# Performance work log

Hardware: AMD Instinct MI355X
Metric: run time of the kernel (lower is better)

## Reference

```python
import jax, jax.numpy as jnp
import numpy as np
import math

B, M, V, C, HID, BIN, H, W = 2, 1024, 300, 128, 128, 256, 384, 512


def fibonacci_sphere(n):
    # generate_grasp_views: n approximately-uniform directions on the unit sphere
    i = np.arange(n, dtype=np.float64)
    phi = (np.sqrt(5.0) - 1.0) / 2.0
    z = (2.0 * i + 1.0) / n - 1.0
    r = np.sqrt(np.maximum(1.0 - z * z, 0.0))
    t = 2.0 * np.pi * i * phi
    v = np.stack([r * np.cos(t), r * np.sin(t), z], -1)
    return (v / np.linalg.norm(v, axis=-1, keepdims=True)).astype(np.float32)


def setup_inputs():
    key = jax.random.key(0)
    ks = jax.random.split(key, 24)
    seed_features = jax.random.normal(ks[0], (B, C, M), jnp.float32)
    token_sel_idx = jax.random.randint(ks[1], (B, M), 0, H * W)
    fx = 525.0
    Kmat = jnp.array([[fx, 0.0, W / 2.0], [0.0, fx, H / 2.0], [0.0, 0.0, 1.0]], jnp.float32)
    K = jnp.broadcast_to(Kmat, (B, 3, 3))
    depth_map = 0.2 + 0.8 * jax.random.uniform(ks[2], (B, 1, H, W), jnp.float32)
    depth_prob = jax.nn.softmax(jax.random.normal(ks[3], (B, BIN, H, W), jnp.float32), axis=1)
    view_dirs = jnp.asarray(fibonacci_sphere(V))

    def lin(k, fan_in, shape):
        s = 1.0 / np.sqrt(fan_in)
        return jax.random.uniform(k, shape, jnp.float32, -s, s)

    qin = C + 7  # seed_feat + ray(3) + normal(3) + uncert(1)
    params = dict(
        Wq1=lin(ks[4], qin, (qin, HID)), bq1=lin(ks[5], qin, (HID,)),
        Wq2=lin(ks[6], HID, (HID, HID)), bq2=lin(ks[7], HID, (HID,)),
        Wa1=lin(ks[8], 3, (3, HID)), ba1=lin(ks[9], 3, (HID,)),
        Wa2=lin(ks[10], HID, (HID, HID)), ba2=lin(ks[11], HID, (HID,)),
        Wb1=lin(ks[12], 3, (3, HID // 2)), bb1=lin(ks[13], 3, (HID // 2,)),
        Wb2=lin(ks[14], HID // 2, (HID // 2, 1)), bb2=lin(ks[15], HID // 2, (1,)),
        Wr1=lin(ks[16], HID, (HID, C)), br1=lin(ks[17], HID, (C,)),
        Wr2=lin(ks[18], C, (C, C)), br2=lin(ks[19], C, (C,)),
    )
    return dict(seed_features=seed_features, token_sel_idx=token_sel_idx, K=K,
                depth_map=depth_map, depth_prob=depth_prob, view_dirs=view_dirs, **params)


def _views_to_rot(views):
    # batch_viewpoint_params_to_matrix(-views, angle=0)
    axis_x = -views
    zero = jnp.zeros_like(axis_x[..., 0])
    axis_y = jnp.stack([-axis_x[..., 1], axis_x[..., 0], zero], -1)
    ny = jnp.linalg.norm(axis_y, axis=-1, keepdims=True)
    fallback = jnp.broadcast_to(jnp.array([0.0, 1.0, 0.0], views.dtype), axis_y.shape)
    axis_y = jnp.where(ny < 1e-8, fallback, axis_y / jnp.maximum(ny, 1e-8))
    axis_x = axis_x / jnp.maximum(jnp.linalg.norm(axis_x, axis=-1, keepdims=True), 1e-8)
    axis_z = jnp.cross(axis_x, axis_y)
    return jnp.stack([axis_x, axis_y, axis_z], -1)  # (B,M,3,3)


def _forward(seed_features, token_sel_idx, K, depth_map, depth_prob, view_dirs,
             Wq1, bq1, Wq2, bq2, Wa1, ba1, Wa2, ba2, Wb1, bb1, Wb2, bb2, Wr1, br1, Wr2, br2):
    depth_map = jax.lax.stop_gradient(depth_map)   # .detach() in torch
    depth_prob = jax.lax.stop_gradient(depth_prob)
    # --- backproject depth to xyz map (B,3,H,W) ---
    ys, xs = jnp.meshgrid(jnp.arange(H, dtype=jnp.float32), jnp.arange(W, dtype=jnp.float32), indexing='ij')
    fx = K[:, 0, 0][:, None, None, None]; fy = K[:, 1, 1][:, None, None, None]
    cx = K[:, 0, 2][:, None, None, None]; cy = K[:, 1, 2][:, None, None, None]
    z = depth_map
    x = (xs[None, None] - cx) / fx * z
    y = (ys[None, None] - cy) / fy * z
    xyz = jnp.concatenate([x, y, z], axis=1)
    # --- central-difference normal map with replicate pad ---
    dx = (xyz[:, :, :, 2:] - xyz[:, :, :, :-2])[:, :, 1:-1, :]
    dy = (xyz[:, :, 2:, :] - xyz[:, :, :-2, :])[:, :, :, 1:-1]
    n = jnp.cross(dx.transpose(0, 2, 3, 1), dy.transpose(0, 2, 3, 1))
    n = n / jnp.maximum(jnp.linalg.norm(n, axis=-1, keepdims=True), 1e-6)
    normal_map = jnp.pad(n.transpose(0, 3, 1, 2), ((0, 0), (0, 0), (1, 1), (1, 1)), mode='edge')
    # --- depth uncertainty: normalized entropy over bins ---
    p = jnp.maximum(depth_prob, 1e-8)
    uncert_map = jnp.clip(-(p * jnp.log(p)).sum(axis=1, keepdims=True) / math.log(BIN), 0.0, 1.0)
    # --- per-seed irregular gathers ---
    def gather(feat, idx):
        Bf, Cf = feat.shape[0], feat.shape[1]
        flat = feat.reshape(Bf, Cf, H * W)
        return jnp.take_along_axis(flat, jnp.broadcast_to(idx[:, None, :], (Bf, Cf, idx.shape[1])), axis=2)
    normal_bm3 = gather(normal_map, token_sel_idx).transpose(0, 2, 1)  # (B,M,3)
    uncert_bm1 = gather(uncert_map, token_sel_idx).transpose(0, 2, 1)  # (B,M,1)
    u = (token_sel_idx % W).astype(jnp.float32)
    v = (token_sel_idx // W).astype(jnp.float32)
    rx = (u - K[:, 0, 2][:, None]) / K[:, 0, 0][:, None]
    ry = (v - K[:, 1, 2][:, None]) / K[:, 1, 1][:, None]
    rays = jnp.stack([rx, ry, jnp.ones_like(rx)], -1)
    rays = rays / jnp.maximum(jnp.linalg.norm(rays, axis=-1, keepdims=True), 1e-12)
    normal_bm3 = normal_bm3 * (1.0 - uncert_bm1)
    # --- query / anchor / bias MLPs ---
    q_in = jnp.concatenate([seed_features.transpose(0, 2, 1), rays, normal_bm3, uncert_bm1], -1)
    q = jax.nn.relu(jax.nn.relu(q_in @ Wq1 + bq1) @ Wq2 + bq2)          # (B,M,HID)
    a = jax.nn.relu(view_dirs @ Wa1 + ba1) @ Wa2 + ba2                  # (V,HID)
    bias = (jax.nn.relu(view_dirs @ Wb1 + bb1) @ Wb2 + bb2)[:, 0]        # (V,)
    logits = jnp.einsum('bmh,vh->bmv', q, a) / jnp.sqrt(jnp.float32(HID)) + bias
    view_score = jax.nn.sigmoid(logits)                                  # (B,M,V)
    # --- top-1 view selection + gather xyz / rot / anchor feat ---
    top_inds = jnp.argmax(view_score, axis=-1)                           # (B,M)
    top_xyz = view_dirs[top_inds]                                        # (B,M,3)
    rot = _views_to_rot(top_xyz)                                         # (B,M,3,3)
    top_a = a[top_inds]                                                  # (B,M,HID)
    res = jax.nn.relu((q + top_a) @ Wr1 + br1) @ Wr2 + br2               # (B,M,C)
    res_feat = res.transpose(0, 2, 1)                                    # (B,C,M)
    return view_score, top_inds, top_xyz, rot, res_feat


def reference(seed_features, token_sel_idx, K, depth_map, depth_prob, view_dirs,
              Wq1, bq1, Wq2, bq2, Wa1, ba1, Wa2, ba2, Wb1, bb1, Wb2, bb2, Wr1, br1, Wr2, br2):
    return _forward(seed_features, token_sel_idx, K, depth_map, depth_prob, view_dirs,
                    Wq1, bq1, Wq2, bq2, Wa1, ba1, Wa2, ba2, Wb1, bb1, Wb2, bb2, Wr1, br1, Wr2, br2)
```

## Files before the change

kernel.cpp:

```cpp
#include <hip/hip_runtime.h>
#include <math.h>

#define B 2
#define M 1024
#define V 300
#define C 128
#define HID 128
#define BIN 256
#define H 384
#define W 512
#define QIN (C + 7)

__global__ __launch_bounds__(HID) void anchor_kernel(
    const float* __restrict__ view_dirs,
    const float* __restrict__ Wa1, const float* __restrict__ ba1,
    const float* __restrict__ Wa2, const float* __restrict__ ba2,
    const float* __restrict__ Wb1, const float* __restrict__ bb1,
    const float* __restrict__ Wb2, const float* __restrict__ bb2,
    float* __restrict__ a_out, float* __restrict__ bias_out) {
  const int v = blockIdx.x;
  const int t = threadIdx.x;
  __shared__ float h1[HID];
  __shared__ float hb[HID / 2];

  const float vd0 = view_dirs[v * 3 + 0];
  const float vd1 = view_dirs[v * 3 + 1];
  const float vd2 = view_dirs[v * 3 + 2];

  float h = vd0 * Wa1[0 * HID + t] + vd1 * Wa1[1 * HID + t] + vd2 * Wa1[2 * HID + t] + ba1[t];
  h1[t] = fmaxf(h, 0.0f);
  if (t < HID / 2) {
    float x = vd0 * Wb1[0 * 64 + t] + vd1 * Wb1[1 * 64 + t] + vd2 * Wb1[2 * 64 + t] + bb1[t];
    hb[t] = fmaxf(x, 0.0f);
  }
  __syncthreads();

  float acc = ba2[t];
#pragma unroll 8
  for (int k = 0; k < HID; ++k) acc += h1[k] * Wa2[k * HID + t];
  a_out[v * HID + t] = acc;

  if (t == 0) {
    float bacc = bb2[0];
    for (int k = 0; k < 64; ++k) bacc += hb[k] * Wb2[k];
    bias_out[v] = bacc;
  }
}

__global__ __launch_bounds__(128) void seed_kernel(
    const float* __restrict__ seed_features, const int* __restrict__ token_sel_idx,
    const float* __restrict__ Kmat, const float* __restrict__ depth_map,
    const float* __restrict__ depth_prob, const float* __restrict__ view_dirs,
    const float* __restrict__ Wq1, const float* __restrict__ bq1,
    const float* __restrict__ Wq2, const float* __restrict__ bq2,
    const float* __restrict__ Wr1, const float* __restrict__ br1,
    const float* __restrict__ Wr2, const float* __restrict__ br2,
    const float* __restrict__ a_ws, const float* __restrict__ bias_ws,
    float* __restrict__ out_view_score, float* __restrict__ out_top_inds,
    float* __restrict__ out_top_xyz, float* __restrict__ out_rot,
    float* __restrict__ out_res) {
  const int bm = blockIdx.x;
  const int b = bm / M;
  const int m = bm - b * M;
  const int t = threadIdx.x;

  __shared__ float qin_s[QIN + 1];
  __shared__ float hs[HID];
  __shared__ float qs[HID];
  __shared__ float red_v[128];
  __shared__ int   red_i[128];
  __shared__ float atop_s[HID];

  qin_s[t] = seed_features[((size_t)b * C + t) * M + m];

  const int idx = token_sel_idx[b * M + m];

  {
    const float* dp = depth_prob + (size_t)b * BIN * H * W + idx;
    float p0 = fmaxf(dp[(size_t)(2 * t + 0) * (H * W)], 1e-8f);
    float p1 = fmaxf(dp[(size_t)(2 * t + 1) * (H * W)], 1e-8f);
    red_v[t] = p0 * logf(p0) + p1 * logf(p1);
  }
  __syncthreads();
  for (int s = 64; s > 0; s >>= 1) {
    if (t < s) red_v[t] += red_v[t + s];
    __syncthreads();
  }

  if (t == 0) {
    float uncert = (-red_v[0]) / 5.5451774444795623f;
    uncert = fminf(fmaxf(uncert, 0.0f), 1.0f);

    const float fx = Kmat[b * 9 + 0], fy = Kmat[b * 9 + 4];
    const float cx = Kmat[b * 9 + 2], cy = Kmat[b * 9 + 5];
    const int w = idx % W;
    const int h = idx / W;
    const int hc = min(max(h, 1), H - 2);
    const int wc = min(max(w, 1), W - 2);

    const float* dm = depth_map + (size_t)b * H * W;
    const float zl = dm[hc * W + (wc - 1)];
    const float zr = dm[hc * W + (wc + 1)];
    const float zu = dm[(hc - 1) * W + wc];
    const float zd = dm[(hc + 1) * W + wc];

    const float dxx = (wc + 1 - cx) / fx * zr - (wc - 1 - cx) / fx * zl;
    const float dxy = (hc - cy) / fy * zr - (hc - cy) / fy * zl;
    const float dxz = zr - zl;
    const float dyx = (wc - cx) / fx * zd - (wc - cx) / fx * zu;
    const float dyy = (hc + 1 - cy) / fy * zd - (hc - 1 - cy) / fy * zu;
    const float dyz = zd - zu;

    float nx = dxy * dyz - dxz * dyy;
    float ny = dxz * dyx - dxx * dyz;
    float nz = dxx * dyy - dxy * dyx;
    const float nn = fmaxf(sqrtf(nx * nx + ny * ny + nz * nz), 1e-6f);
    const float sc = (1.0f - uncert) / nn;

    const float rx = ((float)w - cx) / fx;
    const float ry = ((float)h - cy) / fy;
    const float rn = fmaxf(sqrtf(rx * rx + ry * ry + 1.0f), 1e-12f);

    qin_s[128] = rx / rn;
    qin_s[129] = ry / rn;
    qin_s[130] = 1.0f / rn;
    qin_s[131] = nx * sc;
    qin_s[132] = ny * sc;
    qin_s[133] = nz * sc;
    qin_s[134] = uncert;
  }
  __syncthreads();

  float acc = bq1[t];
#pragma unroll 5
  for (int i = 0; i < QIN; ++i) acc += qin_s[i] * Wq1[i * HID + t];
  hs[t] = fmaxf(acc, 0.0f);
  __syncthreads();

  acc = bq2[t];
#pragma unroll 8
  for (int k = 0; k < HID; ++k) acc += hs[k] * Wq2[k * HID + t];
  qs[t] = fmaxf(acc, 0.0f);
  __syncthreads();

  float bestv = -1.0f;
  int besti = 0;
  float* vs_out = out_view_score + (size_t)bm * V;
  for (int v = t; v < V; v += 128) {
    const float* av = a_ws + v * HID;
    float dot = 0.0f;
#pragma unroll 8
    for (int k = 0; k < HID; ++k) dot += qs[k] * av[k];
    const float logit = dot / sqrtf((float)HID) + bias_ws[v];
    const float scv = 1.0f / (1.0f + expf(-logit));
    vs_out[v] = scv;
    if (scv > bestv) { bestv = scv; besti = v; }
  }
  red_v[t] = bestv;
  red_i[t] = besti;
  __syncthreads();
  for (int s = 64; s > 0; s >>= 1) {
    if (t < s) {
      const float ov = red_v[t + s];
      const int oi = red_i[t + s];
      if (ov > red_v[t] || (ov == red_v[t] && oi < red_i[t])) {
        red_v[t] = ov;
        red_i[t] = oi;
      }
    }
    __syncthreads();
  }
  const int best = red_i[0];

  if (t == 0) {
    out_top_inds[bm] = (float)best;
    const float vx = view_dirs[best * 3 + 0];
    const float vy = view_dirs[best * 3 + 1];
    const float vz = view_dirs[best * 3 + 2];
    out_top_xyz[(size_t)bm * 3 + 0] = vx;
    out_top_xyz[(size_t)bm * 3 + 1] = vy;
    out_top_xyz[(size_t)bm * 3 + 2] = vz;

    float ax0 = -vx, ax1 = -vy, ax2 = -vz;
    float ay0 = vy, ay1 = -vx, ay2 = 0.0f;
    const float nyn = sqrtf(ay0 * ay0 + ay1 * ay1);
    if (nyn < 1e-8f) {
      ay0 = 0.0f; ay1 = 1.0f; ay2 = 0.0f;
    } else {
      const float d = fmaxf(nyn, 1e-8f);
      ay0 /= d; ay1 /= d;
    }
    const float an = fmaxf(sqrtf(ax0 * ax0 + ax1 * ax1 + ax2 * ax2), 1e-8f);
    ax0 /= an; ax1 /= an; ax2 /= an;
    const float az0 = ax1 * ay2 - ax2 * ay1;
    const float az1 = ax2 * ay0 - ax0 * ay2;
    const float az2 = ax0 * ay1 - ax1 * ay0;
    float* R = out_rot + (size_t)bm * 9;
    R[0] = ax0; R[1] = ay0; R[2] = az0;
    R[3] = ax1; R[4] = ay1; R[5] = az1;
    R[6] = ax2; R[7] = ay2; R[8] = az2;
  }

  atop_s[t] = a_ws[best * HID + t];
  __syncthreads();

  float racc = br1[t];
#pragma unroll 8
  for (int k = 0; k < HID; ++k) racc += (qs[k] + atop_s[k]) * Wr1[k * HID + t];
  hs[t] = fmaxf(racc, 0.0f);
  __syncthreads();

  racc = br2[t];
#pragma unroll 8
  for (int k = 0; k < HID; ++k) racc += hs[k] * Wr2[k * HID + t];
  out_res[((size_t)b * C + t) * M + m] = racc;
}

extern "C" void kernel_launch(void* const* d_in, const int* in_sizes, int n_in,
                              void* d_out, int out_size, void* d_ws, size_t ws_size,
                              hipStream_t stream) {
  const float* seed  = (const float*)d_in[0];
  const int*   tok   = (const int*)d_in[1];
  const float* Km    = (const float*)d_in[2];
  const float* dmap  = (const float*)d_in[3];
  const float* dprob = (const float*)d_in[4];
  const float* vdirs = (const float*)d_in[5];
  const float* Wq1 = (const float*)d_in[6];  const float* bq1 = (const float*)d_in[7];
  const float* Wq2 = (const float*)d_in[8];  const float* bq2 = (const float*)d_in[9];
  const float* Wa1 = (const float*)d_in[10]; const float* ba1 = (const float*)d_in[11];
  const float* Wa2 = (const float*)d_in[12]; const float* ba2 = (const float*)d_in[13];
  const float* Wb1 = (const float*)d_in[14]; const float* bb1 = (const float*)d_in[15];
  const float* Wb2 = (const float*)d_in[16]; const float* bb2 = (const float*)d_in[17];
  const float* Wr1 = (const float*)d_in[18]; const float* br1 = (const float*)d_in[19];
  const float* Wr2 = (const float*)d_in[20]; const float* br2 = (const float*)d_in[21];

  float* out = (float*)d_out;
  float* vs  = out;
  float* ti  = vs + (size_t)B * M * V;
  float* tx  = ti + (size_t)B * M;
  float* rot = tx + (size_t)B * M * 3;
  float* rf  = rot + (size_t)B * M * 9;

  float* a_ws    = (float*)d_ws;
  float* bias_ws = a_ws + (size_t)V * HID;

  anchor_kernel<<<V, HID, 0, stream>>>(vdirs, Wa1, ba1, Wa2, ba2, Wb1, bb1, Wb2, bb2,
                                       a_ws, bias_ws);
  seed_kernel<<<B * M, 128, 0, stream>>>(seed, tok, Km, dmap, dprob, vdirs,
                                         Wq1, bq1, Wq2, bq2, Wr1, br1, Wr2, br2,
                                         a_ws, bias_ws, vs, ti, tx, rot, rf);
}
```

Before: 568.4 us.

## Transpose anchor and seed layouts for coalesced loads, use wave-shuffle reductions

Stores a transposed copy of the anchor features so each thread computes three view logits with coalesced reads across views, replacing the strided per-view dot products. Adds a pre-transpose kernel so seed features are read contiguously per token. Replaces the shared-memory tree reductions for entropy and argmax with wavefront shuffles plus a two-wave combine, and fuses the bias MLP reduction into a shuffle. This adds a transpose kernel launch and extra workspace, and the padded third column is clamped to stay in bounds.

```diff
diff --git a/kernel.cpp b/kernel.cpp
--- a/kernel.cpp
+++ b/kernel.cpp
@@ -11,17 +11,33 @@
 #define W 512
 #define QIN (C + 7)
 
+__global__ __launch_bounds__(128) void transpose_seed(
+    const float* __restrict__ in, float* __restrict__ out) {
+  __shared__ float tile[32][33];
+  const int b  = blockIdx.z;
+  const int c0 = blockIdx.x * 32;
+  const int m0 = blockIdx.y * 32;
+  const int tx = threadIdx.x;
+#pragma unroll
+  for (int r = threadIdx.y; r < 32; r += 4)
+    tile[r][tx] = in[((size_t)b * C + c0 + r) * M + m0 + tx];
+  __syncthreads();
+#pragma unroll
+  for (int r = threadIdx.y; r < 32; r += 4)
+    out[((size_t)b * M + m0 + r) * C + c0 + tx] = tile[tx][r];
+}
+
 __global__ __launch_bounds__(HID) void anchor_kernel(
     const float* __restrict__ view_dirs,
     const float* __restrict__ Wa1, const float* __restrict__ ba1,
     const float* __restrict__ Wa2, const float* __restrict__ ba2,
     const float* __restrict__ Wb1, const float* __restrict__ bb1,
     const float* __restrict__ Wb2, const float* __restrict__ bb2,
-    float* __restrict__ a_out, float* __restrict__ bias_out) {
+    float* __restrict__ a_out, float* __restrict__ aT_out,
+    float* __restrict__ bias_out) {
   const int v = blockIdx.x;
   const int t = threadIdx.x;
   __shared__ float h1[HID];
-  __shared__ float hb[HID / 2];
 
   const float vd0 = view_dirs[v * 3 + 0];
   const float vd1 = view_dirs[v * 3 + 1];
@@ -29,9 +45,13 @@
 
   float h = vd0 * Wa1[0 * HID + t] + vd1 * Wa1[1 * HID + t] + vd2 * Wa1[2 * HID + t] + ba1[t];
   h1[t] = fmaxf(h, 0.0f);
-  if (t < HID / 2) {
+
+  if (t < 64) {
     float x = vd0 * Wb1[0 * 64 + t] + vd1 * Wb1[1 * 64 + t] + vd2 * Wb1[2 * 64 + t] + bb1[t];
-    hb[t] = fmaxf(x, 0.0f);
+    x = fmaxf(x, 0.0f) * Wb2[t];
+#pragma unroll
+    for (int o = 32; o > 0; o >>= 1) x += __shfl_down(x, o, 64);
+    if (t == 0) bias_out[v] = x + bb2[0];
   }
   __syncthreads();
 
@@ -39,23 +59,19 @@
 #pragma unroll 8
   for (int k = 0; k < HID; ++k) acc += h1[k] * Wa2[k * HID + t];
   a_out[v * HID + t] = acc;
-
-  if (t == 0) {
-    float bacc = bb2[0];
-    for (int k = 0; k < 64; ++k) bacc += hb[k] * Wb2[k];
-    bias_out[v] = bacc;
-  }
+  aT_out[(size_t)t * V + v] = acc;
 }
 
 __global__ __launch_bounds__(128) void seed_kernel(
-    const float* __restrict__ seed_features, const int* __restrict__ token_sel_idx,
+    const float* __restrict__ seedT, const int* __restrict__ token_sel_idx,
     const float* __restrict__ Kmat, const float* __restrict__ depth_map,
     const float* __restrict__ depth_prob, const float* __restrict__ view_dirs,
     const float* __restrict__ Wq1, const float* __restrict__ bq1,
     const float* __restrict__ Wq2, const float* __restrict__ bq2,
     const float* __restrict__ Wr1, const float* __restrict__ br1,
     const float* __restrict__ Wr2, const float* __restrict__ br2,
-    const float* __restrict__ a_ws, const float* __restrict__ bias_ws,
+    const float* __restrict__ a_ws, const float* __restrict__ aT_ws,
+    const float* __restrict__ bias_ws,
     float* __restrict__ out_view_score, float* __restrict__ out_top_inds,
     float* __restrict__ out_top_xyz, float* __restrict__ out_rot,
     float* __restrict__ out_res) {
@@ -63,15 +79,19 @@
   const int b = bm / M;
   const int m = bm - b * M;
   const int t = threadIdx.x;
+  const int lane = t & 63;
+  const int wv = t >> 6;
 
   __shared__ float qin_s[QIN + 1];
   __shared__ float hs[HID];
   __shared__ float qs[HID];
-  __shared__ float red_v[128];
-  __shared__ int   red_i[128];
   __shared__ float atop_s[HID];
-
-  qin_s[t] = seed_features[((size_t)b * C + t) * M + m];
+  __shared__ float ered[2];
+  __shared__ float wbv[2];
+  __shared__ int   wbi[2];
+  __shared__ int   sbest;
+
+  qin_s[t] = seedT[((size_t)b * M + m) * C + t];
 
   const int idx = token_sel_idx[b * M + m];
 
@@ -79,16 +99,15 @@
     const float* dp = depth_prob + (size_t)b * BIN * H * W + idx;
     float p0 = fmaxf(dp[(size_t)(2 * t + 0) * (H * W)], 1e-8f);
     float p1 = fmaxf(dp[(size_t)(2 * t + 1) * (H * W)], 1e-8f);
-    red_v[t] = p0 * logf(p0) + p1 * logf(p1);
-  }
-  __syncthreads();
-  for (int s = 64; s > 0; s >>= 1) {
-    if (t < s) red_v[t] += red_v[t + s];
-    __syncthreads();
-  }
+    float e = p0 * logf(p0) + p1 * logf(p1);
+#pragma unroll
+    for (int o = 32; o > 0; o >>= 1) e += __shfl_down(e, o, 64);
+    if (lane == 0) ered[wv] = e;
+  }
+  __syncthreads();
 
   if (t == 0) {
-    float uncert = (-red_v[0]) / 5.5451774444795623f;
+    float uncert = (-(ered[0] + ered[1])) / 5.5451774444795623f;
     uncert = fminf(fmaxf(uncert, 0.0f), 1.0f);
 
     const float fx = Kmat[b * 9 + 0], fy = Kmat[b * 9 + 4];
@@ -143,40 +162,47 @@
   qs[t] = fmaxf(acc, 0.0f);
   __syncthreads();
 
-  float bestv = -1.0f;
-  int besti = 0;
+  const int col2 = 256 + (t < 44 ? t : 43);
+  float d0 = 0.0f, d1 = 0.0f, d2 = 0.0f;
+#pragma unroll 8
+  for (int k = 0; k < HID; ++k) {
+    const float qk = qs[k];
+    const float* row = aT_ws + (size_t)k * V;
+    d0 += qk * row[t];
+    d1 += qk * row[t + 128];
+    d2 += qk * row[col2];
+  }
+  const float rsq = 0.08838834764831845f;
+  const float sc0 = 1.0f / (1.0f + expf(-(d0 * rsq + bias_ws[t])));
+  const float sc1 = 1.0f / (1.0f + expf(-(d1 * rsq + bias_ws[t + 128])));
+  const float sc2 = 1.0f / (1.0f + expf(-(d2 * rsq + bias_ws[col2])));
+
   float* vs_out = out_view_score + (size_t)bm * V;
-  for (int v = t; v < V; v += 128) {
-    const float* av = a_ws + v * HID;
-    float dot = 0.0f;
-#pragma unroll 8
-    for (int k = 0; k < HID; ++k) dot += qs[k] * av[k];
-    const float logit = dot / sqrtf((float)HID) + bias_ws[v];
-    const float scv = 1.0f / (1.0f + expf(-logit));
-    vs_out[v] = scv;
-    if (scv > bestv) { bestv = scv; besti = v; }
-  }
-  red_v[t] = bestv;
-  red_i[t] = besti;
-  __syncthreads();
-  for (int s = 64; s > 0; s >>= 1) {
-    if (t < s) {
-      const float ov = red_v[t + s];
-      const int oi = red_i[t + s];
-      if (ov > red_v[t] || (ov == red_v[t] && oi < red_i[t])) {
-        red_v[t] = ov;
-        red_i[t] = oi;
-      }
-    }
-    __syncthreads();
-  }
-  const int best = red_i[0];
+  vs_out[t] = sc0;
+  vs_out[t + 128] = sc1;
+  if (t < 44) vs_out[t + 256] = sc2;
+
+  float bv = sc0; int bi = t;
+  if (sc1 > bv) { bv = sc1; bi = t + 128; }
+  if (t < 44 && sc2 > bv) { bv = sc2; bi = t + 256; }
+#pragma unroll
+  for (int o = 32; o > 0; o >>= 1) {
+    const float ov = __shfl_down(bv, o, 64);
+    const int oi = __shfl_down(bi, o, 64);
+    if (ov > bv || (ov == bv && oi < bi)) { bv = ov; bi = oi; }
+  }
+  if (lane == 0) { wbv[wv] = bv; wbi[wv] = bi; }
+  __syncthreads();
 
   if (t == 0) {
-    out_top_inds[bm] = (float)best;
-    const float vx = view_dirs[best * 3 + 0];
-    const float vy = view_dirs[best * 3 + 1];
-    const float vz = view_dirs[best * 3 + 2];
+    float fbv = wbv[0]; int fbi = wbi[0];
+    if (wbv[1] > fbv || (wbv[1] == fbv && wbi[1] < fbi)) { fbv = wbv[1]; fbi = wbi[1]; }
+    sbest = fbi;
+
+    out_top_inds[bm] = (float)fbi;
+    const float vx = view_dirs[fbi * 3 + 0];
+    const float vy = view_dirs[fbi * 3 + 1];
+    const float vz = view_dirs[fbi * 3 + 2];
     out_top_xyz[(size_t)bm * 3 + 0] = vx;
     out_top_xyz[(size_t)bm * 3 + 1] = vy;
     out_top_xyz[(size_t)bm * 3 + 2] = vz;
@@ -200,6 +226,8 @@
     R[3] = ax1; R[4] = ay1; R[5] = az1;
     R[6] = ax2; R[7] = ay2; R[8] = az2;
   }
+  __syncthreads();
+  const int best = sbest;
 
   atop_s[t] = a_ws[best * HID + t];
   __syncthreads();
@@ -242,11 +270,14 @@
   float* rf  = rot + (size_t)B * M * 9;
 
   float* a_ws    = (float*)d_ws;
-  float* bias_ws = a_ws + (size_t)V * HID;
-
+  float* aT_ws   = a_ws + (size_t)V * HID;
+  float* bias_ws = aT_ws + (size_t)HID * V;
+  float* seedT   = bias_ws + V;
+
+  transpose_seed<<<dim3(C / 32, M / 32, B), dim3(32, 4), 0, stream>>>(seed, seedT);
   anchor_kernel<<<V, HID, 0, stream>>>(vdirs, Wa1, ba1, Wa2, ba2, Wb1, bb1, Wb2, bb2,
-                                       a_ws, bias_ws);
-  seed_kernel<<<B * M, 128, 0, stream>>>(seed, tok, Km, dmap, dprob, vdirs,
+                                       a_ws, aT_ws, bias_ws);
+  seed_kernel<<<B * M, 128, 0, stream>>>(seedT, tok, Km, dmap, dprob, vdirs,
                                          Wq1, bq1, Wq2, bq2, Wr1, br1, Wr2, br2,
-                                         a_ws, bias_ws, vs, ti, tx, rot, rf);
-}
+                                         a_ws, aT_ws, bias_ws, vs, ti, tx, rot, rf);
+}
```

Result: faster. 550.3 us (-3.2%).
